# Kernel optimization log

Measured on AMD Instinct MI355X. Metric: run time of the kernel, lower is better.

Reference implementation:

```python
import jax, jax.numpy as jnp
import numpy as np
import math

DIM = 512
WINDOW = 4
TOPK = 8


def setup_inputs() -> dict:
    key = jax.random.key(0)
    ks = jax.random.split(key, 14)
    B, N, D = 4, 4096, DIM
    s = 0.02
    return {
        'mu':  jax.random.normal(ks[0], (B, N, D), jnp.float32),
        'Wq':  jax.random.normal(ks[1], (D, D), jnp.float32) * s,
        'bq':  jnp.zeros((D,), jnp.float32),
        'Wk':  jax.random.normal(ks[2], (D, D), jnp.float32) * s,
        'bk':  jnp.zeros((D,), jnp.float32),
        'Wv':  jax.random.normal(ks[3], (D, D), jnp.float32) * s,
        'bv':  jnp.zeros((D,), jnp.float32),
        'Wm1': jax.random.normal(ks[4], (2 * D, D), jnp.float32) * s,
        'bm1': jnp.zeros((D,), jnp.float32),
        'Wm2': jax.random.normal(ks[5], (D, D), jnp.float32) * s,
        'bm2': jnp.zeros((D,), jnp.float32),
        'Wo':  jax.random.normal(ks[6], (2 * D, D), jnp.float32) * s,
        'bo':  jnp.zeros((D,), jnp.float32),
    }


def reference(mu, Wq, bq, Wk, bk, Wv, bv, Wm1, bm1, Wm2, bm2, Wo, bo):
    B, N, D = mu.shape
    W = WINDOW
    # ---- local windowed message passing ----
    padded = jnp.pad(mu, ((0, 0), (W, 0), (0, 0)))  # left-pad seq with W zeros
    # neighbors[:, n, w-1] = mu[:, n-w] (zeros if n-w < 0); [B, N, W, D]
    neighbors = jnp.stack([padded[:, W - w:W - w + N, :] for w in range(1, W + 1)], axis=2)
    self_exp = jnp.broadcast_to(mu[:, :, None, :], neighbors.shape)
    h = jnp.concatenate([self_exp, neighbors], axis=-1)  # [B, N, W, 2D]
    h = jax.nn.silu(h @ Wm1 + bm1)
    local_msgs = (h @ Wm2 + bm2).mean(axis=2)  # [B, N, D]
    # ---- sparse causal global attention ----
    q = mu @ Wq + bq
    k = mu @ Wk + bk
    v = mu @ Wv + bv
    scores = jnp.einsum('bnd,bmd->bnm', q, k) * (1.0 / math.sqrt(D))
    causal = jnp.tril(jnp.ones((N, N), bool))
    scores = jnp.where(causal, scores, -jnp.inf)
    # top-k then softmax over kept entries == softmax over scatter(-inf elsewhere)
    topk_vals, topk_idx = jax.lax.top_k(scores, TOPK)  # [B, N, K]
    probs = jax.nn.softmax(topk_vals, axis=-1)
    bi = jnp.arange(B)[:, None, None]
    ni = jnp.arange(N)[None, :, None]
    attn = jnp.zeros_like(scores).at[bi, ni, topk_idx].set(probs)  # [B, N, N]
    global_msgs = jnp.einsum('bnm,bmd->bnd', attn, v)
    return jnp.concatenate([local_msgs, global_msgs], axis=-1) @ Wo + bo
```

## Files before the change

kernel.cpp:

```cpp
#include <hip/hip_runtime.h>
#include <math.h>

#define DIM 512
#define NSEQ 4096
#define BATCH 4
#define ROWS (BATCH * NSEQ)

typedef unsigned long long u64;
typedef unsigned int u32;
typedef unsigned short u16;
typedef __attribute__((ext_vector_type(8))) short bf16x8;
typedef __attribute__((ext_vector_type(4))) float f32x4;

__device__ __forceinline__ u32 to_bf16(float f) {
  u32 x = __float_as_uint(f);
  return (x + 0x7fffu + ((x >> 16) & 1u)) >> 16;
}
__device__ __forceinline__ u32 pk2(float a, float b) {
  return to_bf16(a) | (to_bf16(b) << 16);
}
__device__ __forceinline__ uint4 pk8(float4 a, float4 b) {
  return make_uint4(pk2(a.x, a.y), pk2(a.z, a.w), pk2(b.x, b.y), pk2(b.z, b.w));
}

__device__ __forceinline__ void insert_top8(u64 (&a)[8], u64 key) {
  if (key <= a[7]) return;
  a[7] = key;
#pragma unroll
  for (int i = 7; i > 0; --i) {
    u64 x = a[i - 1], y = a[i];
    u64 hi = x > y ? x : y;
    u64 lo = x > y ? y : x;
    a[i - 1] = hi;
    a[i] = lo;
  }
}
template<int NN>
__device__ __forceinline__ void insert_topN(u64 (&a)[NN], u64 key) {
  if (key <= a[NN - 1]) return;
  a[NN - 1] = key;
#pragma unroll
  for (int i = NN - 1; i > 0; --i) {
    u64 x = a[i - 1], y = a[i];
    u64 hi = x > y ? x : y;
    u64 lo = x > y ? y : x;
    a[i - 1] = hi;
    a[i] = lo;
  }
}
__device__ __forceinline__ float decode_val(u64 key) {
  u32 ord = (u32)(key >> 32);
  u32 s = (ord & 0x80000000u) ? (ord ^ 0x80000000u) : ~ord;
  return __uint_as_float(s);
}
__device__ __forceinline__ u64 pack_key(float v, int m) {
  u32 sb = __float_as_uint(v);
  u32 ord = sb ^ ((sb >> 31) ? 0xFFFFFFFFu : 0x80000000u);
  return ((u64)ord << 32) | (u32)(~(u32)m);
}

__device__ __forceinline__ int fbal(int sub) {
  const int g = sub >> 5, i = sub & 31;
  return (g == 0) ? i : (g == 1) ? (63 - i) : (g == 2) ? (64 + i) : (127 - i);
}

__global__ __launch_bounds__(256) void gemm64qk(const float* __restrict__ mu,
                                                const float* __restrict__ Wq,
                                                const float* __restrict__ bq,
                                                const float* __restrict__ Wk,
                                                const float* __restrict__ bk,
                                                float* __restrict__ Q,
                                                float* __restrict__ Kf,
                                                u16* __restrict__ Kc) {
  __shared__ float As[16][132];
  __shared__ float Bs[16][132];
  const int tid = threadIdx.x;
  const int tx = tid & 15, ty = tid >> 4;
  const int bx = blockIdx.x;
  const bool isK = bx >= 4;
  const int n0 = (bx & 3) * 128;
  const int m0 = blockIdx.y * 128;
  const float* W = isK ? Wk : Wq;
  const float* bias = isK ? bk : bq;
  float* C = isK ? Kf : Q;
  const int arow = tid >> 1, ah8 = (tid & 1) * 8;
  const int bkk = tid >> 4, bc8 = (tid & 15) * 8;
  float acc[8][8] = {};
  for (int k0 = 0; k0 < DIM; k0 += 16) {
    float4 a0 = *(const float4*)(mu + (size_t)(m0 + arow) * DIM + (k0 + ah8));
    float4 a1 = *(const float4*)(mu + (size_t)(m0 + arow) * DIM + (k0 + ah8 + 4));
    float4 b0 = *(const float4*)(W + (size_t)(k0 + bkk) * DIM + (n0 + bc8));
    float4 b1 = *(const float4*)(W + (size_t)(k0 + bkk) * DIM + (n0 + bc8 + 4));
    As[ah8 + 0][arow] = a0.x; As[ah8 + 1][arow] = a0.y;
    As[ah8 + 2][arow] = a0.z; As[ah8 + 3][arow] = a0.w;
    As[ah8 + 4][arow] = a1.x; As[ah8 + 5][arow] = a1.y;
    As[ah8 + 6][arow] = a1.z; As[ah8 + 7][arow] = a1.w;
    *(float4*)&Bs[bkk][bc8] = b0;
    *(float4*)&Bs[bkk][bc8 + 4] = b1;
    __syncthreads();
#pragma unroll
    for (int kk = 0; kk < 16; ++kk) {
      float4 av0 = *(const float4*)&As[kk][ty * 8];
      float4 av1 = *(const float4*)&As[kk][ty * 8 + 4];
      float4 bv0 = *(const float4*)&Bs[kk][tx * 8];
      float4 bv1 = *(const float4*)&Bs[kk][tx * 8 + 4];
      float a8[8] = {av0.x, av0.y, av0.z, av0.w, av1.x, av1.y, av1.z, av1.w};
      float b8[8] = {bv0.x, bv0.y, bv0.z, bv0.w, bv1.x, bv1.y, bv1.z, bv1.w};
#pragma unroll
      for (int i = 0; i < 8; ++i)
#pragma unroll
        for (int j = 0; j < 8; ++j)
          acc[i][j] = fmaf(a8[i], b8[j], acc[i][j]);
    }
    __syncthreads();
  }
  float4 bb0 = *(const float4*)(bias + n0 + tx * 8);
  float4 bb1 = *(const float4*)(bias + n0 + tx * 8 + 4);
#pragma unroll
  for (int i = 0; i < 8; ++i) {
    int row = m0 + ty * 8 + i;
#pragma unroll
    for (int jb = 0; jb < 2; ++jb) {
      int col = n0 + tx * 8 + jb * 4;
      float4 bb = jb ? bb1 : bb0;
      float4 o;
      o.x = acc[i][jb * 4 + 0] + bb.x;
      o.y = acc[i][jb * 4 + 1] + bb.y;
      o.z = acc[i][jb * 4 + 2] + bb.z;
      o.w = acc[i][jb * 4 + 3] + bb.w;
      *(float4*)(C + (size_t)row * DIM + col) = o;
      if (isK) {
        int batch = row >> 12, key = row & 4095;
        int kt = key >> 6, kl = key & 63;
        int chunk = col >> 5;
        size_t didx = ((size_t)batch << 21) +
                      ((size_t)((kt * 16 + chunk) * 64 + kl)) * 32 + (col & 31);
        *(uint2*)(Kc + didx) = make_uint2(pk2(o.x, o.y), pk2(o.z, o.w));
      }
    }
  }
}

__global__ __launch_bounds__(256) void wtrans6(const float* __restrict__ Wv,
                                               const float* __restrict__ Wm1,
                                               const float* __restrict__ Wm2,
                                               const float* __restrict__ Wo,
                                               u16* __restrict__ WT) {
  const size_t DD = (size_t)DIM * DIM;
  const int y = blockIdx.y;
  const float* src = (y == 0) ? Wv
                   : (y == 1) ? Wm1
                   : (y == 2) ? Wm1 + DD
                   : (y == 3) ? Wm2
                   : (y == 4) ? Wo
                              : Wo + DD;
  u16* dst = WT + (size_t)y * DD;
  int o = blockIdx.x * 256 + threadIdx.x;
  int n = o >> 7;
  int k0 = (o & 127) * 4;
  float a0 = src[(size_t)(k0 + 0) * DIM + n];
  float a1 = src[(size_t)(k0 + 1) * DIM + n];
  float a2 = src[(size_t)(k0 + 2) * DIM + n];
  float a3 = src[(size_t)(k0 + 3) * DIM + n];
  ((uint2*)dst)[(n << 7) + (k0 >> 2)] = make_uint2(pk2(a0, a1), pk2(a2, a3));
}

__global__ __launch_bounds__(256) void wtrans1(const float* __restrict__ src,
                                               u16* __restrict__ dst) {
  int o = blockIdx.x * 256 + threadIdx.x;
  int n = o >> 7;
  int k0 = (o & 127) * 4;
  float a0 = src[(size_t)(k0 + 0) * DIM + n];
  float a1 = src[(size_t)(k0 + 1) * DIM + n];
  float a2 = src[(size_t)(k0 + 2) * DIM + n];
  float a3 = src[(size_t)(k0 + 3) * DIM + n];
  ((uint2*)dst)[(n << 7) + (k0 >> 2)] = make_uint2(pk2(a0, a1), pk2(a2, a3));
}

__global__ void bcomb_k(const float* __restrict__ bm2, const float* __restrict__ Wo,
                        const float* __restrict__ bo, float* __restrict__ bc) {
  int c = blockIdx.x * 256 + threadIdx.x;
  if (c >= DIM) return;
  float s = bo[c];
  for (int k = 0; k < DIM; ++k) s = fmaf(bm2[k], Wo[(size_t)k * DIM + c], s);
  bc[c] = s;
}

__global__ __launch_bounds__(256) void gemmbf(const float* __restrict__ A, int lda,
                                              const u16* __restrict__ WT,
                                              const float* __restrict__ bias,
                                              float* C, int ldc, int accum) {
  __shared__ u16 As[128 * 32];
  __shared__ u16 Bs[128 * 32];
  const int tid = threadIdx.x;
  const int n0 = blockIdx.x * 128;
  const int m0 = blockIdx.y * 128;
  const int l = tid & 63, lr = l & 15, lu = l >> 4;
  const int wid = tid >> 6, wr = wid >> 1, wc = wid & 1;
  const int srow = tid >> 1, shalf = tid & 1;
  f32x4 acc[4][4] = {};
  for (int k0 = 0; k0 < 512; k0 += 32) {
    __syncthreads();
    {
      const float4* a4 = (const float4*)(A + (size_t)(m0 + srow) * lda + k0 + shalf * 16);
      float4 u0 = a4[0], u1 = a4[1], u2 = a4[2], u3 = a4[3];
      int sw = (srow >> 1) & 3;
      *(uint4*)&As[srow * 32 + ((shalf * 2 + 0) ^ sw) * 8] = pk8(u0, u1);
      *(uint4*)&As[srow * 32 + ((shalf * 2 + 1) ^ sw) * 8] = pk8(u2, u3);
    }
    {
      const uint4* b4 = (const uint4*)(WT + (size_t)(n0 + srow) * 512 + k0 + shalf * 16);
      uint4 v0 = b4[0], v1 = b4[1];
      int sw = (srow >> 1) & 3;
      *(uint4*)&Bs[srow * 32 + ((shalf * 2 + 0) ^ sw) * 8] = v0;
      *(uint4*)&Bs[srow * 32 + ((shalf * 2 + 1) ^ sw) * 8] = v1;
    }
    __syncthreads();
    bf16x8 af[4], bf_[4];
#pragma unroll
    for (int fr = 0; fr < 4; ++fr) {
      int row = wr * 64 + fr * 16 + lr;
      af[fr] = *(const bf16x8*)&As[row * 32 + (lu ^ ((row >> 1) & 3)) * 8];
    }
#pragma unroll
    for (int fc = 0; fc < 4; ++fc) {
      int col = wc * 64 + fc * 16 + lr;
      bf_[fc] = *(const bf16x8*)&Bs[col * 32 + (lu ^ ((col >> 1) & 3)) * 8];
    }
#pragma unroll
    for (int fr = 0; fr < 4; ++fr)
#pragma unroll
      for (int fc = 0; fc < 4; ++fc)
        acc[fr][fc] = __builtin_amdgcn_mfma_f32_16x16x32_bf16(af[fr], bf_[fc], acc[fr][fc], 0, 0, 0);
  }
#pragma unroll
  for (int fr = 0; fr < 4; ++fr)
#pragma unroll
    for (int fc = 0; fc < 4; ++fc) {
      int col = n0 + wc * 64 + fc * 16 + lr;
      float bb = bias ? bias[col] : 0.f;
#pragma unroll
      for (int j = 0; j < 4; ++j) {
        int row = m0 + wr * 64 + fr * 16 + lu * 4 + j;
        size_t off = (size_t)row * ldc + col;
        float o = acc[fr][fc][j] + bb;
        if (accum) o += C[off];
        C[off] = o;
      }
    }
}

__global__ __launch_bounds__(256) void silu_combine(const float* P,
                                                    const float* bm1,
                                                    float* Gout) {
  size_t idx = (size_t)blockIdx.x * 256 + threadIdx.x;
  int r = (int)(idx >> 7);
  int c4 = (int)(idx & 127);
  int n = r & (NSEQ - 1);
  const float4* P4 = (const float4*)P;
  float4 a = P4[(size_t)r * 256 + c4];
  float4 bm = ((const float4*)bm1)[c4];
  float bx = a.x + bm.x, by = a.y + bm.y, bz = a.z + bm.z, bw = a.w + bm.w;
  float sx = 0.f, sy = 0.f, sz = 0.f, sw = 0.f;
#pragma unroll
  for (int w = 1; w <= 4; ++w) {
    float ex = bx, ey = by, ez = bz, ew = bw;
    if (n >= w) {
      float4 nb = P4[(size_t)(r - w) * 256 + 128 + c4];
      ex += nb.x; ey += nb.y; ez += nb.z; ew += nb.w;
    }
    sx += ex / (1.f + expf(-ex));
    sy += ey / (1.f + expf(-ey));
    sz += ez / (1.f + expf(-ez));
    sw += ew / (1.f + expf(-ew));
  }
  ((float4*)Gout)[(size_t)r * 128 + c4] =
      make_float4(0.25f * sx, 0.25f * sy, 0.25f * sz, 0.25f * sw);
}

__global__ __launch_bounds__(256, 4) void attn_fused(const float* __restrict__ Qf,
                                                     const float* __restrict__ Kf,
                                                     const u16* __restrict__ Kc,
                                                     const float* __restrict__ V,
                                                     float* __restrict__ G) {
  __shared__ union UA {
    struct { u16 Qs[16 * 512]; u64 cand[256][8]; } s;
    float Qf32[16][512];
  } uA;
  __shared__ int cidx[16][16];
  __shared__ u64 exkey[16][16];
  __shared__ float psm[16][8];
  __shared__ int pidx[16][8];

  const int tid = threadIdx.x;
  const int bid = blockIdx.x;
  const int xcd = bid & 7;
  const int b = xcd >> 1;
  const int par = xcd & 1;
  const int sub = bid >> 3;
  const int qt = 2 * fbal(sub) + par;
  const int n0 = qt * 16;
  const size_t rb = (size_t)b * NSEQ;
  const float SCALE_F = 0.04419417382415922f;

  const int l = tid & 63, lr = l & 15, lu = l >> 4;
  const int wid = tid >> 6;
  const int mbase = lu * 4;

  {
    int row = tid >> 4, part = tid & 15;
    const float4* src = (const float4*)(Qf + ((rb + n0 + row) << 9));
#pragma unroll
    for (int c = 0; c < 4; ++c) {
      int slot = part * 4 + c;
      float4 x = src[slot * 2], y = src[slot * 2 + 1];
      *(uint4*)&uA.s.Qs[row * 512 + (slot ^ (row & 7)) * 8] = pk8(x, y);
    }
  }
  __syncthreads();

  u64 best[8] = {};
  const int nq = n0 + lr;

  const int nkt = (n0 + 16 + 63) >> 6;
  const int lo = (lr * 32) + lu * 8;
  for (int kt = wid; kt < nkt; kt += 4) {
    const int m0 = kt << 6;
    const u16* kb = Kc + ((size_t)b << 21) + (size_t)kt * 32768;
    f32x4 acc[4] = {};
    bf16x8 kcur[4], knxt[4];
#pragma unroll
    for (int fk = 0; fk < 4; ++fk)
      kcur[fk] = *(const bf16x8*)(kb + fk * 512 + lo);
#pragma unroll
    for (int ks = 0; ks < 16; ++ks) {
      if (ks < 15) {
        const u16* cb = kb + (ks + 1) * 2048;
#pragma unroll
        for (int fk = 0; fk < 4; ++fk)
          knxt[fk] = *(const bf16x8*)(cb + fk * 512 + lo);
      }
      bf16x8 qf = *(const bf16x8*)&uA.s.Qs[lr * 512 + ((ks * 4 + lu) ^ (lr & 7)) * 8];
#pragma unroll
      for (int fk = 0; fk < 4; ++fk)
        acc[fk] = __builtin_amdgcn_mfma_f32_16x16x32_bf16(kcur[fk], qf, acc[fk], 0, 0, 0);
      if (ks < 15) {
#pragma unroll
        for (int fk = 0; fk < 4; ++fk) kcur[fk] = knxt[fk];
      }
    }
    if (m0 + 63 <= n0) {
#pragma unroll
      for (int fk = 0; fk < 4; ++fk)
#pragma unroll
        for (int j = 0; j < 4; ++j)
          insert_top8(best, pack_key(acc[fk][j], m0 + fk * 16 + mbase + j));
    } else {
#pragma unroll
      for (int fk = 0; fk < 4; ++fk)
#pragma unroll
        for (int j = 0; j < 4; ++j) {
          int m = m0 + fk * 16 + mbase + j;
          if (m <= nq) insert_top8(best, pack_key(acc[fk][j], m));
        }
    }
  }

  __syncthreads();
#pragma unroll
  for (int i = 0; i < 8; ++i) uA.s.cand[tid][i] = best[i];
  __syncthreads();

  if (tid < 16) {
    u64 mb[16] = {};
    for (int w = 0; w < 4; ++w)
      for (int u = 0; u < 4; ++u) {
        const u64* cl = uA.s.cand[w * 64 + u * 16 + tid];
#pragma unroll
        for (int i = 0; i < 8; ++i) insert_topN<16>(mb, cl[i]);
      }
#pragma unroll
    for (int i = 0; i < 16; ++i)
      cidx[tid][i] = (mb[i] != 0ULL) ? (int)(~(u32)mb[i]) : -1;
  }
  __syncthreads();

  {
    int row = tid >> 4, seg = tid & 15;
    const float4* src = (const float4*)(Qf + ((rb + n0 + row) << 9));
    float4* dst = (float4*)&uA.Qf32[row][0];
#pragma unroll
    for (int c = 0; c < 8; ++c) dst[seg * 8 + c] = src[seg * 8 + c];
  }
  __syncthreads();

  {
    const int g = tid >> 2;
    const int lsub = tid & 3;
    const int qi = g >> 2;
    const int cblk = g & 3;
    const float4* q4 = (const float4*)&uA.Qf32[qi][0];
#pragma unroll
    for (int cc = 0; cc < 4; ++cc) {
      int c = cblk * 4 + cc;
      int ci = cidx[qi][c];
      float4 p = make_float4(0.f, 0.f, 0.f, 0.f);
      if (ci >= 0) {
        const float4* k4 = (const float4*)(Kf + ((rb + ci) << 9));
#pragma unroll 8
        for (int t = 0; t < 32; ++t) {
          float4 kv = k4[4 * t + lsub];
          float4 qv = q4[4 * t + lsub];
          p.x = fmaf(kv.x, qv.x, p.x);
          p.y = fmaf(kv.y, qv.y, p.y);
          p.z = fmaf(kv.z, qv.z, p.z);
          p.w = fmaf(kv.w, qv.w, p.w);
        }
      }
      p.x += __shfl_xor(p.x, 2);
      p.y += __shfl_xor(p.y, 2);
      p.z += __shfl_xor(p.z, 2);
      p.w += __shfl_xor(p.w, 2);
      p.x += __shfl_xor(p.x, 1);
      p.y += __shfl_xor(p.y, 1);
      p.z += __shfl_xor(p.z, 1);
      p.w += __shfl_xor(p.w, 1);
      float rx = p.x + p.z;
      float ry = p.y + p.w;
      float r = rx + ry;
      if (lsub == 0)
        exkey[qi][c] = (ci >= 0) ? pack_key(r * SCALE_F, ci) : 0ULL;
    }
  }
  __syncthreads();

  if (tid < 16) {
    u64 mb[8] = {};
#pragma unroll
    for (int t2 = 0; t2 < 16; ++t2) insert_top8(mb, exkey[tid][t2]);
    float vmax = decode_val(mb[0]);
    float e[8];
#pragma unroll
    for (int i = 0; i < 8; ++i)
      e[i] = (mb[i] != 0ULL) ? expf(decode_val(mb[i]) - vmax) : 0.f;
    float s01 = e[0] + e[1], s23 = e[2] + e[3];
    float s45 = e[4] + e[5], s67 = e[6] + e[7];
    float ssum = (s01 + s23) + (s45 + s67);
#pragma unroll
    for (int i = 0; i < 8; ++i) {
      psm[tid][i] = e[i] / ssum;
      pidx[tid][i] = (mb[i] != 0ULL) ? (int)(~(u32)mb[i]) : 0;
    }
  }
  __syncthreads();

  {
    const int qi = tid >> 4, seg = tid & 15;
    float pp[8];
    int ix[8];
#pragma unroll
    for (int i = 0; i < 8; ++i) { pp[i] = psm[qi][i]; ix[i] = pidx[qi][i]; }
    const float4* V4 = (const float4*)V;
    float4* G4 = (float4*)G;
    const size_t ob = ((rb + n0 + qi) << 7) + seg * 8;
#pragma unroll
    for (int it = 0; it < 8; ++it) {
      float4 a = make_float4(0.f, 0.f, 0.f, 0.f);
#pragma unroll
      for (int i = 0; i < 8; ++i) {
        float4 vv = V4[((rb + ix[i]) << 7) + seg * 8 + it];
        a.x = fmaf(pp[i], vv.x, a.x);
        a.y = fmaf(pp[i], vv.y, a.y);
        a.z = fmaf(pp[i], vv.z, a.z);
        a.w = fmaf(pp[i], vv.w, a.w);
      }
      G4[ob + it] = a;
    }
  }
}

extern "C" void kernel_launch(void* const* d_in, const int* in_sizes, int n_in,
                              void* d_out, int out_size, void* d_ws, size_t ws_size,
                              hipStream_t stream) {
  const float* mu = (const float*)d_in[0];
  const float* Wq = (const float*)d_in[1];
  const float* bq = (const float*)d_in[2];
  const float* Wk = (const float*)d_in[3];
  const float* bk = (const float*)d_in[4];
  const float* Wv = (const float*)d_in[5];
  const float* bv = (const float*)d_in[6];
  const float* Wm1 = (const float*)d_in[7];
  const float* bm1 = (const float*)d_in[8];
  const float* Wm2 = (const float*)d_in[9];
  const float* bm2 = (const float*)d_in[10];
  const float* Wo = (const float*)d_in[11];
  const float* bo = (const float*)d_in[12];
  float* out = (float*)d_out;

  float* ws = (float*)d_ws;
  const size_t RD = (size_t)ROWS * DIM;
  const size_t DD = (size_t)DIM * DIM;
  float* X1 = ws;
  float* X2 = X1 + RD;
  float* X3 = X2 + RD;
  float* X4 = X3 + RD;
  u16* Kc = (u16*)(X4 + RD);
  u16* WT = Kc + RD;
  u16* WvT = WT;
  u16* Wm1aT = WT + DD;
  u16* WoTT = WT + 4 * DD;
  u16* WoBT = WT + 5 * DD;
  float* Wcombf = (float*)(WT + 6 * DD);
  u16* WcombT = (u16*)(Wcombf + DD);
  float* bcomb = (float*)(WcombT + DD);

  dim3 blk(256);
  dim3 gqk(8, ROWS / 128);
  dim3 gbf(DIM / 128, ROWS / 128);
  dim3 gbf2(2 * DIM / 128, ROWS / 128);

  wtrans6<<<dim3(256, 6), blk, 0, stream>>>(Wv, Wm1, Wm2, Wo, WT);

  gemmbf<<<dim3(4, 4), blk, 0, stream>>>(Wm2, 512, WoTT, (const float*)nullptr, Wcombf, 512, 0);
  bcomb_k<<<dim3(2), blk, 0, stream>>>(bm2, Wo, bo, bcomb);
  wtrans1<<<dim3(256), blk, 0, stream>>>(Wcombf, WcombT);

  gemm64qk<<<gqk, blk, 0, stream>>>(mu, Wq, bq, Wk, bk, X1, X2, Kc);

  gemmbf<<<gbf, blk, 0, stream>>>(mu, 512, WvT, bv, X3, 512, 0);

  attn_fused<<<dim3(1024), blk, 0, stream>>>(X1, X2, Kc, X3, X4);

  gemmbf<<<gbf2, blk, 0, stream>>>(mu, 512, Wm1aT, (const float*)nullptr, X1, 1024, 0);
  silu_combine<<<dim3(ROWS * 128 / 256), blk, 0, stream>>>(X1, bm1, X3);

  gemmbf<<<gbf, blk, 0, stream>>>(X3, 512, WcombT, bcomb, out, 512, 0);
  gemmbf<<<gbf, blk, 0, stream>>>(X4, 512, WoBT, (const float*)nullptr, out, 512, 1);
}
```

Baseline: 741.3 us.

## Feed bf16 activations to gemmbf and load tiles with direct global-to-LDS copies

The bf16 GEMM now takes bf16 A operands: mu is converted once inside the QK GEMM, and silu_combine and attention write their outputs as bf16 instead of fp32. Tiles are staged with global_load_lds direct copies, which drops the register round trip and the XOR swizzle, and a Wm2 bf16 copy is added to the weight-prep kernel. This halves A-side read traffic and cuts conversion work in every gemmbf launch. The cost is possible LDS bank conflicts from the unswizzled layout, plus extra writes in the QK GEMM.

```diff
diff --git a/kernel.cpp b/kernel.cpp
--- a/kernel.cpp
+++ b/kernel.cpp
@@ -11,6 +11,9 @@
 typedef unsigned short u16;
 typedef __attribute__((ext_vector_type(8))) short bf16x8;
 typedef __attribute__((ext_vector_type(4))) float f32x4;
+
+typedef const __attribute__((address_space(1))) void* gas1;
+typedef __attribute__((address_space(3))) void* las3;
 
 __device__ __forceinline__ u32 to_bf16(float f) {
   u32 x = __float_as_uint(f);
@@ -71,7 +74,8 @@
                                                 const float* __restrict__ bk,
                                                 float* __restrict__ Q,
                                                 float* __restrict__ Kf,
-                                                u16* __restrict__ Kc) {
+                                                u16* __restrict__ Kc,
+                                                u16* __restrict__ Mu16) {
   __shared__ float As[16][132];
   __shared__ float Bs[16][132];
   const int tid = threadIdx.x;
@@ -91,6 +95,8 @@
     float4 a1 = *(const float4*)(mu + (size_t)(m0 + arow) * DIM + (k0 + ah8 + 4));
     float4 b0 = *(const float4*)(W + (size_t)(k0 + bkk) * DIM + (n0 + bc8));
     float4 b1 = *(const float4*)(W + (size_t)(k0 + bkk) * DIM + (n0 + bc8 + 4));
+    if (bx == 0)
+      *(uint4*)(Mu16 + (size_t)(m0 + arow) * DIM + k0 + ah8) = pk8(a0, a1);
     As[ah8 + 0][arow] = a0.x; As[ah8 + 1][arow] = a0.y;
     As[ah8 + 2][arow] = a0.z; As[ah8 + 3][arow] = a0.w;
     As[ah8 + 4][arow] = a1.x; As[ah8 + 5][arow] = a1.y;
@@ -141,21 +147,26 @@
   }
 }
 
-__global__ __launch_bounds__(256) void wtrans6(const float* __restrict__ Wv,
+__global__ __launch_bounds__(256) void wtrans7(const float* __restrict__ Wv,
                                                const float* __restrict__ Wm1,
                                                const float* __restrict__ Wm2,
                                                const float* __restrict__ Wo,
                                                u16* __restrict__ WT) {
   const size_t DD = (size_t)DIM * DIM;
   const int y = blockIdx.y;
+  u16* dst = WT + (size_t)y * DD;
+  int o = blockIdx.x * 256 + threadIdx.x;
+  if (y == 6) {
+    const float* s = Wm2 + (size_t)o * 4;
+    ((uint2*)dst)[o] = make_uint2(pk2(s[0], s[1]), pk2(s[2], s[3]));
+    return;
+  }
   const float* src = (y == 0) ? Wv
                    : (y == 1) ? Wm1
                    : (y == 2) ? Wm1 + DD
                    : (y == 3) ? Wm2
                    : (y == 4) ? Wo
                               : Wo + DD;
-  u16* dst = WT + (size_t)y * DD;
-  int o = blockIdx.x * 256 + threadIdx.x;
   int n = o >> 7;
   int k0 = (o & 127) * 4;
   float a0 = src[(size_t)(k0 + 0) * DIM + n];
@@ -186,10 +197,10 @@
   bc[c] = s;
 }
 
-__global__ __launch_bounds__(256) void gemmbf(const float* __restrict__ A, int lda,
-                                              const u16* __restrict__ WT,
-                                              const float* __restrict__ bias,
-                                              float* C, int ldc, int accum) {
+__global__ __launch_bounds__(256, 4) void gemmbf(const u16* __restrict__ A, int lda,
+                                                 const u16* __restrict__ WT,
+                                                 const float* __restrict__ bias,
+                                                 float* C, int ldc, int accum) {
   __shared__ u16 As[128 * 32];
   __shared__ u16 Bs[128 * 32];
   const int tid = threadIdx.x;
@@ -197,35 +208,29 @@
   const int m0 = blockIdx.y * 128;
   const int l = tid & 63, lr = l & 15, lu = l >> 4;
   const int wid = tid >> 6, wr = wid >> 1, wc = wid & 1;
-  const int srow = tid >> 1, shalf = tid & 1;
+  const int lrow = l >> 2, lseg = (l & 3) * 8;
   f32x4 acc[4][4] = {};
   for (int k0 = 0; k0 < 512; k0 += 32) {
     __syncthreads();
-    {
-      const float4* a4 = (const float4*)(A + (size_t)(m0 + srow) * lda + k0 + shalf * 16);
-      float4 u0 = a4[0], u1 = a4[1], u2 = a4[2], u3 = a4[3];
-      int sw = (srow >> 1) & 3;
-      *(uint4*)&As[srow * 32 + ((shalf * 2 + 0) ^ sw) * 8] = pk8(u0, u1);
-      *(uint4*)&As[srow * 32 + ((shalf * 2 + 1) ^ sw) * 8] = pk8(u2, u3);
-    }
-    {
-      const uint4* b4 = (const uint4*)(WT + (size_t)(n0 + srow) * 512 + k0 + shalf * 16);
-      uint4 v0 = b4[0], v1 = b4[1];
-      int sw = (srow >> 1) & 3;
-      *(uint4*)&Bs[srow * 32 + ((shalf * 2 + 0) ^ sw) * 8] = v0;
-      *(uint4*)&Bs[srow * 32 + ((shalf * 2 + 1) ^ sw) * 8] = v1;
+#pragma unroll
+    for (int j = 0; j < 2; ++j) {
+      int r0 = wid * 32 + j * 16;
+      const u16* sa = A + (size_t)(m0 + r0 + lrow) * lda + k0 + lseg;
+      const u16* sb = WT + (size_t)(n0 + r0 + lrow) * 512 + k0 + lseg;
+      __builtin_amdgcn_global_load_lds((gas1)sa, (las3)&As[r0 * 32], 16, 0, 0);
+      __builtin_amdgcn_global_load_lds((gas1)sb, (las3)&Bs[r0 * 32], 16, 0, 0);
     }
     __syncthreads();
     bf16x8 af[4], bf_[4];
 #pragma unroll
     for (int fr = 0; fr < 4; ++fr) {
       int row = wr * 64 + fr * 16 + lr;
-      af[fr] = *(const bf16x8*)&As[row * 32 + (lu ^ ((row >> 1) & 3)) * 8];
+      af[fr] = *(const bf16x8*)&As[row * 32 + lu * 8];
     }
 #pragma unroll
     for (int fc = 0; fc < 4; ++fc) {
       int col = wc * 64 + fc * 16 + lr;
-      bf_[fc] = *(const bf16x8*)&Bs[col * 32 + (lu ^ ((col >> 1) & 3)) * 8];
+      bf_[fc] = *(const bf16x8*)&Bs[col * 32 + lu * 8];
     }
 #pragma unroll
     for (int fr = 0; fr < 4; ++fr)
@@ -252,7 +257,7 @@
 
 __global__ __launch_bounds__(256) void silu_combine(const float* P,
                                                     const float* bm1,
-                                                    float* Gout) {
+                                                    u16* Gout16) {
   size_t idx = (size_t)blockIdx.x * 256 + threadIdx.x;
   int r = (int)(idx >> 7);
   int c4 = (int)(idx & 127);
@@ -274,15 +279,15 @@
     sz += ez / (1.f + expf(-ez));
     sw += ew / (1.f + expf(-ew));
   }
-  ((float4*)Gout)[(size_t)r * 128 + c4] =
-      make_float4(0.25f * sx, 0.25f * sy, 0.25f * sz, 0.25f * sw);
+  *(uint2*)(Gout16 + (size_t)r * 512 + c4 * 4) =
+      make_uint2(pk2(0.25f * sx, 0.25f * sy), pk2(0.25f * sz, 0.25f * sw));
 }
 
 __global__ __launch_bounds__(256, 4) void attn_fused(const float* __restrict__ Qf,
                                                      const float* __restrict__ Kf,
                                                      const u16* __restrict__ Kc,
                                                      const float* __restrict__ V,
-                                                     float* __restrict__ G) {
+                                                     u16* __restrict__ G) {
   __shared__ union UA {
     struct { u16 Qs[16 * 512]; u64 cand[256][8]; } s;
     float Qf32[16][512];
@@ -461,8 +466,7 @@
 #pragma unroll
     for (int i = 0; i < 8; ++i) { pp[i] = psm[qi][i]; ix[i] = pidx[qi][i]; }
     const float4* V4 = (const float4*)V;
-    float4* G4 = (float4*)G;
-    const size_t ob = ((rb + n0 + qi) << 7) + seg * 8;
+    u16* Gb = G + ((size_t)(rb + n0 + qi)) * 512 + seg * 32;
 #pragma unroll
     for (int it = 0; it < 8; ++it) {
       float4 a = make_float4(0.f, 0.f, 0.f, 0.f);
@@ -474,7 +478,7 @@
         a.z = fmaf(pp[i], vv.z, a.z);
         a.w = fmaf(pp[i], vv.w, a.w);
       }
-      G4[ob + it] = a;
+      *(uint2*)(Gb + it * 4) = make_uint2(pk2(a.x, a.y), pk2(a.z, a.w));
     }
   }
 }
@@ -510,30 +514,32 @@
   u16* Wm1aT = WT + DD;
   u16* WoTT = WT + 4 * DD;
   u16* WoBT = WT + 5 * DD;
-  float* Wcombf = (float*)(WT + 6 * DD);
+  u16* Wm216 = WT + 6 * DD;
+  float* Wcombf = (float*)(WT + 7 * DD);
   u16* WcombT = (u16*)(Wcombf + DD);
   float* bcomb = (float*)(WcombT + DD);
+  u16* Mu16 = (u16*)(bcomb + 512);
 
   dim3 blk(256);
   dim3 gqk(8, ROWS / 128);
   dim3 gbf(DIM / 128, ROWS / 128);
   dim3 gbf2(2 * DIM / 128, ROWS / 128);
 
-  wtrans6<<<dim3(256, 6), blk, 0, stream>>>(Wv, Wm1, Wm2, Wo, WT);
-
-  gemmbf<<<dim3(4, 4), blk, 0, stream>>>(Wm2, 512, WoTT, (const float*)nullptr, Wcombf, 512, 0);
+  wtrans7<<<dim3(256, 7), blk, 0, stream>>>(Wv, Wm1, Wm2, Wo, WT);
+
+  gemmbf<<<dim3(4, 4), blk, 0, stream>>>(Wm216, 512, WoTT, (const float*)nullptr, Wcombf, 512, 0);
   bcomb_k<<<dim3(2), blk, 0, stream>>>(bm2, Wo, bo, bcomb);
   wtrans1<<<dim3(256), blk, 0, stream>>>(Wcombf, WcombT);
 
-  gemm64qk<<<gqk, blk, 0, stream>>>(mu, Wq, bq, Wk, bk, X1, X2, Kc);
-
-  gemmbf<<<gbf, blk, 0, stream>>>(mu, 512, WvT, bv, X3, 512, 0);
-
-  attn_fused<<<dim3(1024), blk, 0, stream>>>(X1, X2, Kc, X3, X4);
-
-  gemmbf<<<gbf2, blk, 0, stream>>>(mu, 512, Wm1aT, (const float*)nullptr, X1, 1024, 0);
-  silu_combine<<<dim3(ROWS * 128 / 256), blk, 0, stream>>>(X1, bm1, X3);
-
-  gemmbf<<<gbf, blk, 0, stream>>>(X3, 512, WcombT, bcomb, out, 512, 0);
-  gemmbf<<<gbf, blk, 0, stream>>>(X4, 512, WoBT, (const float*)nullptr, out, 512, 1);
-}
+  gemm64qk<<<gqk, blk, 0, stream>>>(mu, Wq, bq, Wk, bk, X1, X2, Kc, Mu16);
+
+  gemmbf<<<gbf, blk, 0, stream>>>(Mu16, 512, WvT, bv, X3, 512, 0);
+
+  attn_fused<<<dim3(1024), blk, 0, stream>>>(X1, X2, Kc, X3, (u16*)X4);
+
+  gemmbf<<<gbf2, blk, 0, stream>>>(Mu16, 512, Wm1aT, (const float*)nullptr, X1, 1024, 0);
+  silu_combine<<<dim3(ROWS * 128 / 256), blk, 0, stream>>>(X1, bm1, (u16*)X3);
+
+  gemmbf<<<gbf, blk, 0, stream>>>((u16*)X3, 512, WcombT, bcomb, out, 512, 0);
+  gemmbf<<<gbf, blk, 0, stream>>>((u16*)X4, 512, WoBT, (const float*)nullptr, out, 512, 1);
+}
```

Measured after the change: 697.4 us. 1.06x faster.
